# Kernel tuning notes

Measured on AMD Instinct MI355X. Metric: run time of the kernel, lower is better.

Reference implementation:

```python
import jax, jax.numpy as jnp
import numpy as np

B, T, C = 1, 2048, 1024
H, D = 16, 64  # n_head, head_size (n_query_groups == n_head -> plain MHA)


def build_rope_cache(seq_len, n_elem, base=10000):
    theta = 1.0 / (base ** (jnp.arange(0, n_elem, 2, dtype=jnp.float32) / n_elem))
    idx_theta = jnp.outer(jnp.arange(seq_len, dtype=jnp.float32), theta)
    idx_theta = jnp.concatenate([idx_theta, idx_theta], axis=-1)  # torch .repeat(1, 2)
    return jnp.cos(idx_theta), jnp.sin(idx_theta)


def apply_rope(x, cos, sin):
    d = x.shape[-1]
    x1, x2 = x[..., : d // 2], x[..., d // 2 :]
    rotated = jnp.concatenate([-x2, x1], axis=-1)
    return x * cos + rotated * sin


def fastmax_attention(q, k, v):
    """Fastmax: first-order Taylor approx of softmax attention, causal, O(n*d^2).
    score(i,j) = 1 + q_i . k_j (temperature=1, zero RPE, no dropout);
    out_i = sum_{j<=i} score*v_j / sum_{j<=i} score, via causal cumulative sums."""
    n = q.shape[2]
    kcum = jnp.cumsum(k, axis=2)                                       # (B,H,T,D)
    kvcum = jnp.cumsum(jnp.einsum('bhnd,bhne->bhnde', k, v), axis=2)   # (B,H,T,D,D)
    den = jnp.arange(1, n + 1, dtype=q.dtype) + jnp.einsum('bhnd,bhnd->bhn', q, kcum)
    num = jnp.cumsum(v, axis=2) + jnp.einsum('bhnd,bhnde->bhne', q, kvcum)
    return num / den[..., None]


def setup_inputs() -> dict:
    key = jax.random.key(0)
    k1, k2, k3 = jax.random.split(key, 3)
    scale = 0.02
    x = jax.random.normal(k1, (B, T, C), dtype=jnp.float32)
    w_attn = jax.random.normal(k2, (3 * H * D, C), dtype=jnp.float32) * scale
    w_proj = jax.random.normal(k3, (C, H * D), dtype=jnp.float32) * scale
    cos, sin = build_rope_cache(T, D)
    return {"x": x, "w_attn": w_attn, "w_proj": w_proj, "cos": cos, "sin": sin}


def reference(x, w_attn, w_proj, cos, sin):
    Bx, Tx, Cx = x.shape
    qkv = x @ w_attn.T                                  # (B,T,3HD)
    qkv = qkv.reshape(Bx, Tx, H, 3, D).transpose(0, 2, 3, 1, 4)  # (B,H,3,T,D)
    q, k, v = qkv[:, :, 0], qkv[:, :, 1], qkv[:, :, 2]
    q = apply_rope(q, cos, sin)
    k = apply_rope(k, cos, sin)
    y = fastmax_attention(q, k, v)                      # (B,H,T,D)
    y = y.transpose(0, 2, 1, 3).reshape(Bx, Tx, H * D)
    return y @ w_proj.T
```

## Files before the change

### kernel.cpp

```cpp
#include <hip/hip_runtime.h>

#define T_LEN 2048
#define C_DIM 1024
#define H_NUM 16
#define D_DIM 64
#define QKV_N (3 * H_NUM * D_DIM)
#define L_CHK 64
#define NC (T_LEN / L_CHK)

typedef _Float16 h8 __attribute__((ext_vector_type(8)));
typedef _Float16 h4 __attribute__((ext_vector_type(4)));
typedef float f32x4 __attribute__((ext_vector_type(4)));

__global__ __launch_bounds__(256) void split3_f16(
    const float* __restrict__ x, _Float16* __restrict__ xh,
    _Float16* __restrict__ xl, const float* __restrict__ wa,
    _Float16* __restrict__ wah, _Float16* __restrict__ wal,
    const float* __restrict__ wp, _Float16* __restrict__ wph) {
  int i = (blockIdx.x * 256 + threadIdx.x) * 8;
  const float* src;
  _Float16 *dh, *dl = nullptr;
  int base;
  if (i < 2097152) {
    src = x; dh = xh; dl = xl; base = i;
  } else if (i < 2097152 + 3145728) {
    src = wa; dh = wah; dl = wal; base = i - 2097152;
  } else {
    src = wp; dh = wph; base = i - 5242880;
  }
  float4 a = *(const float4*)(src + base);
  float4 b = *(const float4*)(src + base + 4);
  float v[8] = {a.x, a.y, a.z, a.w, b.x, b.y, b.z, b.w};
  h8 hv, lv;
#pragma unroll
  for (int j = 0; j < 8; ++j) {
    float s = v[j] * 64.f;
    _Float16 h = (_Float16)s;
    hv[j] = h;
    lv[j] = (_Float16)(s - (float)h);
  }
  *(h8*)(dh + base) = hv;
  if (dl) *(h8*)(dl + base) = lv;
}

__device__ __forceinline__ void split8(float4 a, float4 b, h8& hi, h8& lo) {
  float v[8] = {a.x, a.y, a.z, a.w, b.x, b.y, b.z, b.w};
#pragma unroll
  for (int m = 0; m < 8; ++m) {
    _Float16 hh = (_Float16)v[m];
    hi[m] = hh;
    lo[m] = (_Float16)(v[m] - (float)hh);
  }
}

template <int BN, bool ROPE, bool SPLIT3>
__global__ __launch_bounds__(256) void gemm_nt_f16(
    const _Float16* __restrict__ Ah, const _Float16* __restrict__ Al,
    const _Float16* __restrict__ Bh, const _Float16* __restrict__ Bl,
    float* __restrict__ C, const float* __restrict__ cosb,
    const float* __restrict__ sinb, _Float16* __restrict__ qh_,
    _Float16* __restrict__ ql_, _Float16* __restrict__ kh_,
    _Float16* __restrict__ kl_, _Float16* __restrict__ kTh_,
    _Float16* __restrict__ kTl_, _Float16* __restrict__ vTh_,
    _Float16* __restrict__ vTl_, int M, int N, int K, float outscale) {
  constexpr int NJ = BN / 32;
  constexpr int NARR = SPLIT3 ? 2 : 1;
  constexpr int GEMM_BYTES = (64 * 64 * 2 + BN * 64 * 2) * NARR;
  constexpr int ROPE_BYTES = ROPE ? (2 * 64 * 64 * 4 + 64 * 64 * 4) : 0;
  constexpr int SMEM_BYTES = GEMM_BYTES > ROPE_BYTES ? GEMM_BYTES : ROPE_BYTES;
  __shared__ __align__(16) char smem[SMEM_BYTES];
  _Float16* sAh = (_Float16*)smem;
  _Float16* sAl = sAh + 64 * 64;
  _Float16* sBh = sAh + 64 * 64 * NARR;
  _Float16* sBl = sBh + BN * 64;
  const int tid = threadIdx.x;
  const int wave = tid >> 6;
  const int lane = tid & 63;
  const int bm = blockIdx.y * 64;
  const int bn = blockIdx.x * BN;
  const int wm = wave >> 1;
  const int wn = wave & 1;
  const int srow = lane >> 3;
  const int sblk = ((lane & 7) ^ srow) * 8;
  const int quad = lane >> 4;
  const int lrow = lane & 15;

  f32x4 acc[2][NJ];
#pragma unroll
  for (int i = 0; i < 2; ++i)
#pragma unroll
    for (int j = 0; j < NJ; ++j) acc[i][j] = (f32x4){0.f, 0.f, 0.f, 0.f};

  for (int k0 = 0; k0 < K; k0 += 64) {
#pragma unroll
    for (int it = 0; it < 2; ++it) {
      const int ch = wave + it * 4;
      const int row = ch * 8 + srow;
      const _Float16* ga = Ah + (size_t)(bm + row) * K + k0 + sblk;
      __builtin_amdgcn_global_load_lds(
          (const __attribute__((address_space(1))) void*)ga,
          (__attribute__((address_space(3))) void*)(sAh + ch * 512), 16, 0, 0);
      if constexpr (SPLIT3) {
        const _Float16* gb = Al + (size_t)(bm + row) * K + k0 + sblk;
        __builtin_amdgcn_global_load_lds(
            (const __attribute__((address_space(1))) void*)gb,
            (__attribute__((address_space(3))) void*)(sAl + ch * 512), 16, 0,
            0);
      }
    }
#pragma unroll
    for (int it = 0; it < BN / 32; ++it) {
      const int ch = wave + it * 4;
      const int row = ch * 8 + srow;
      const _Float16* ga = Bh + (size_t)(bn + row) * K + k0 + sblk;
      __builtin_amdgcn_global_load_lds(
          (const __attribute__((address_space(1))) void*)ga,
          (__attribute__((address_space(3))) void*)(sBh + ch * 512), 16, 0, 0);
      if constexpr (SPLIT3) {
        const _Float16* gb = Bl + (size_t)(bn + row) * K + k0 + sblk;
        __builtin_amdgcn_global_load_lds(
            (const __attribute__((address_space(1))) void*)gb,
            (__attribute__((address_space(3))) void*)(sBl + ch * 512), 16, 0,
            0);
      }
    }
    __syncthreads();
#pragma unroll
    for (int kk = 0; kk < 2; ++kk) {
      h8 ah[2], al[2], bh[NJ], bl[NJ];
#pragma unroll
      for (int i = 0; i < 2; ++i) {
        const int row = wm * 32 + i * 16 + lrow;
        const int ra = row * 64 + (((kk * 4 + quad) ^ (row & 7)) * 8);
        ah[i] = *(const h8*)&sAh[ra];
        if constexpr (SPLIT3) al[i] = *(const h8*)&sAl[ra];
      }
#pragma unroll
      for (int j = 0; j < NJ; ++j) {
        const int row = wn * (BN / 2) + j * 16 + lrow;
        const int rb = row * 64 + (((kk * 4 + quad) ^ (row & 7)) * 8);
        bh[j] = *(const h8*)&sBh[rb];
        if constexpr (SPLIT3) bl[j] = *(const h8*)&sBl[rb];
      }
#pragma unroll
      for (int i = 0; i < 2; ++i)
#pragma unroll
        for (int j = 0; j < NJ; ++j) {
          acc[i][j] = __builtin_amdgcn_mfma_f32_16x16x32_f16(
              ah[i], bh[j], acc[i][j], 0, 0, 0);
          if constexpr (SPLIT3) {
            acc[i][j] = __builtin_amdgcn_mfma_f32_16x16x32_f16(
                ah[i], bl[j], acc[i][j], 0, 0, 0);
            acc[i][j] = __builtin_amdgcn_mfma_f32_16x16x32_f16(
                al[i], bh[j], acc[i][j], 0, 0, 0);
          }
        }
    }
    __syncthreads();
  }
  if constexpr (!ROPE) {
#pragma unroll
    for (int i = 0; i < 2; ++i) {
      const int rbase = bm + wm * 32 + i * 16 + quad * 4;
#pragma unroll
      for (int j = 0; j < NJ; ++j) {
        const int col = bn + wn * (BN / 2) + j * 16 + lrow;
#pragma unroll
        for (int r = 0; r < 4; ++r)
          C[(size_t)(rbase + r) * N + col] = acc[i][j][r] * outscale;
      }
    }
  } else {
    float* cs = (float*)smem;
    float* sn = cs + 4096;
    float* bounce = sn + 4096;
#pragma unroll
    for (int m = 0; m < 4; ++m) {
      int el = (tid + m * 256) * 4;
      *(float4*)&cs[el] = *(const float4*)&cosb[bm * D_DIM + el];
      *(float4*)&sn[el] = *(const float4*)&sinb[bm * D_DIM + el];
    }
    __syncthreads();
    const int colbase = bn + wn * 64;
    const int type = (colbase >> 6) % 3;
    const int head = colbase / 192;
    const size_t hb = (size_t)head * T_LEN * D_DIM;
    float fv[2][4][4];
#pragma unroll
    for (int i = 0; i < 2; ++i)
#pragma unroll
      for (int r = 0; r < 4; ++r) {
        const int tloc = wm * 32 + i * 16 + quad * 4 + r;
#pragma unroll
        for (int j = 0; j < 4; ++j) {
          const int d = j * 16 + lrow;
          float val = acc[i][j][r] * outscale;
          if (type < 2) {
            float rotv =
                ((j < 2) ? -acc[i][j + 2][r] : acc[i][j - 2][r]) * outscale;
            val = val * cs[tloc * D_DIM + d] + rotv * sn[tloc * D_DIM + d];
          }
          fv[i][r][j] = val;
        }
      }
    if (type < 2) {
      _Float16* dh = (type == 0 ? qh_ : kh_) + hb;
      _Float16* dl = (type == 0 ? ql_ : kl_) + hb;
#pragma unroll
      for (int i = 0; i < 2; ++i)
#pragma unroll
        for (int r = 0; r < 4; ++r) {
          const size_t trow =
              (size_t)(bm + wm * 32 + i * 16 + quad * 4 + r) * D_DIM;
#pragma unroll
          for (int j = 0; j < 4; ++j) {
            const int d = j * 16 + lrow;
            float f = fv[i][r][j];
            _Float16 hh = (_Float16)f;
            dh[trow + d] = hh;
            dl[trow + d] = (_Float16)(f - (float)hh);
          }
        }
    }
    const bool doT = (type >= 1);
    _Float16* th = (type == 1 ? kTh_ : vTh_) + hb;
    _Float16* tl = (type == 1 ? kTl_ : vTl_) + hb;
#pragma unroll
    for (int half = 0; half < 2; ++half) {
      __syncthreads();
      if (wn == half && doT) {
#pragma unroll
        for (int i = 0; i < 2; ++i)
#pragma unroll
          for (int r = 0; r < 4; ++r) {
            const int tloc = wm * 32 + i * 16 + quad * 4 + r;
#pragma unroll
            for (int j = 0; j < 4; ++j) {
              const int d = j * 16 + lrow;
              bounce[tloc * 64 + (d ^ tloc)] = fv[i][r][j];
            }
          }
      }
      __syncthreads();
      if (wn == half && doT) {
        const int lt = wm * 64 + lane;
        const int e = lt >> 1;
        const int tg0 = (lt & 1) * 32;
#pragma unroll
        for (int s8 = 0; s8 < 4; ++s8) {
          h8 hv, lv;
#pragma unroll
          for (int s = 0; s < 8; ++s) {
            const int t = tg0 + s8 * 8 + s;
            float f = bounce[t * 64 + (e ^ t)];
            _Float16 hh = (_Float16)f;
            hv[s] = hh;
            lv[s] = (_Float16)(f - (float)hh);
          }
          *(h8*)&th[(size_t)e * T_LEN + bm + tg0 + s8 * 8] = hv;
          *(h8*)&tl[(size_t)e * T_LEN + bm + tg0 + s8 * 8] = lv;
        }
      }
    }
  }
}

__global__ __launch_bounds__(256) void chunk_kvT(
    const _Float16* __restrict__ kTh, const _Float16* __restrict__ kTl,
    const _Float16* __restrict__ vTh, const _Float16* __restrict__ vTl,
    float* __restrict__ kvchunk, float* __restrict__ kschunk,
    float* __restrict__ vschunk) {
  const int blk = blockIdx.x;
  const int h = blk / NC, c = blk % NC;
  const int tid = threadIdx.x;
  const int wave = tid >> 6, lane = tid & 63;
  const int quad = lane >> 4, lrow = lane & 15;
  const size_t hb = (size_t)h * D_DIM * T_LEN;
  const int tb = c * L_CHK;
  h8 avh[2], avl[2];
  {
    const _Float16* pa = vTh + hb + (size_t)(wave * 16 + lrow) * T_LEN + tb +
                         quad * 8;
    const _Float16* pal = vTl + hb + (size_t)(wave * 16 + lrow) * T_LEN + tb +
                          quad * 8;
    avh[0] = *(const h8*)pa;
    avh[1] = *(const h8*)(pa + 32);
    avl[0] = *(const h8*)pal;
    avl[1] = *(const h8*)(pal + 32);
  }
  f32x4 accv[4];
#pragma unroll
  for (int dt = 0; dt < 4; ++dt) accv[dt] = (f32x4){0.f, 0.f, 0.f, 0.f};
#pragma unroll
  for (int dt = 0; dt < 4; ++dt) {
    const _Float16* pb = kTh + hb + (size_t)(dt * 16 + lrow) * T_LEN + tb +
                         quad * 8;
    const _Float16* pbl = kTl + hb + (size_t)(dt * 16 + lrow) * T_LEN + tb +
                          quad * 8;
#pragma unroll
    for (int ks = 0; ks < 2; ++ks) {
      h8 bh = *(const h8*)(pb + ks * 32);
      h8 bl = *(const h8*)(pbl + ks * 32);
      accv[dt] = __builtin_amdgcn_mfma_f32_16x16x32_f16(avh[ks], bh, accv[dt],
                                                        0, 0, 0);
      accv[dt] = __builtin_amdgcn_mfma_f32_16x16x32_f16(avh[ks], bl, accv[dt],
                                                        0, 0, 0);
      accv[dt] = __builtin_amdgcn_mfma_f32_16x16x32_f16(avl[ks], bh, accv[dt],
                                                        0, 0, 0);
    }
  }
  float* ob = kvchunk + (size_t)blk * (D_DIM * D_DIM);
#pragma unroll
  for (int dt = 0; dt < 4; ++dt)
#pragma unroll
    for (int r = 0; r < 4; ++r)
      ob[(wave * 16 + quad * 4 + r) * D_DIM + dt * 16 + lrow] = accv[dt][r];
  if (tid < 64) {
    const _Float16* p = kTh + hb + (size_t)tid * T_LEN + tb;
    const _Float16* pl = kTl + hb + (size_t)tid * T_LEN + tb;
    float s = 0.f;
#pragma unroll
    for (int i = 0; i < 8; ++i) {
      h8 a = *(const h8*)(p + i * 8), b = *(const h8*)(pl + i * 8);
#pragma unroll
      for (int m = 0; m < 8; ++m) s += (float)a[m] + (float)b[m];
    }
    kschunk[(size_t)blk * D_DIM + tid] = s;
  } else if (tid < 128) {
    const int e = tid - 64;
    const _Float16* p = vTh + hb + (size_t)e * T_LEN + tb;
    const _Float16* pl = vTl + hb + (size_t)e * T_LEN + tb;
    float s = 0.f;
#pragma unroll
    for (int i = 0; i < 8; ++i) {
      h8 a = *(const h8*)(p + i * 8), b = *(const h8*)(pl + i * 8);
#pragma unroll
      for (int m = 0; m < 8; ++m) s += (float)a[m] + (float)b[m];
    }
    vschunk[(size_t)blk * D_DIM + e] = s;
  }
}

__global__ __launch_bounds__(256) void scan_fused(
    const float* __restrict__ kvchunk, float* __restrict__ kvpref,
    const float* __restrict__ kschunk, const float* __restrict__ vschunk,
    float* __restrict__ kspref, float* __restrict__ vspref) {
  int b = blockIdx.x;
  int tid = threadIdx.x;
  if (b < 256) {
    int gid = b * 256 + tid;
    int h = gid >> 12;
    int de = gid & 4095;
    float vals[NC];
#pragma unroll
    for (int c = 0; c < NC; ++c)
      vals[c] = kvchunk[((size_t)(h * NC + c) << 12) + de];
    float run = 0.f;
#pragma unroll
    for (int c = 0; c < NC; ++c) {
      kvpref[((size_t)(h * NC + c) << 12) + de] = run;
      run += vals[c];
    }
  } else {
    int gid = (b - 256) * 256 + tid;
    int h = gid >> 6, d = gid & 63;
    float kv_[NC], vv_[NC];
#pragma unroll
    for (int c = 0; c < NC; ++c) {
      size_t idx = (size_t)(h * NC + c) * 64 + d;
      kv_[c] = kschunk[idx];
      vv_[c] = vschunk[idx];
    }
    float rk = 0.f, rv = 0.f;
#pragma unroll
    for (int c = 0; c < NC; ++c) {
      size_t idx = (size_t)(h * NC + c) * 64 + d;
      kspref[idx] = rk;
      vspref[idx] = rv;
      rk += kv_[c];
      rv += vv_[c];
    }
  }
}

__global__ __launch_bounds__(256) void attn_mfma(
    const _Float16* __restrict__ qh, const _Float16* __restrict__ ql,
    const _Float16* __restrict__ kh, const _Float16* __restrict__ kl,
    const _Float16* __restrict__ vTh, const _Float16* __restrict__ vTl,
    const float* __restrict__ kvpref, const float* __restrict__ kspref,
    const float* __restrict__ vspref, _Float16* __restrict__ yh) {
  __shared__ __align__(16) _Float16 sS[2][4][16 * 64];
  const int blk = blockIdx.x;
  const int h = blk / NC, c = blk % NC;
  const int tid = threadIdx.x;
  const int wave = tid >> 6, lane = tid & 63;
  const int quad = lane >> 4, lrow = lane & 15;
  const size_t hb = (size_t)h * T_LEN * D_DIM;
  const size_t hbT = (size_t)h * D_DIM * T_LEN;
  const int t0 = c * L_CHK;
  const f32x4 z4 = {0.f, 0.f, 0.f, 0.f};
  h8 aqh[2], aql[2];
  {
    const _Float16* pq =
        qh + hb + (size_t)(t0 + wave * 16 + lrow) * D_DIM + quad * 8;
    const _Float16* pql =
        ql + hb + (size_t)(t0 + wave * 16 + lrow) * D_DIM + quad * 8;
    aqh[0] = *(const h8*)pq;
    aqh[1] = *(const h8*)(pq + 32);
    aql[0] = *(const h8*)pql;
    aql[1] = *(const h8*)(pql + 32);
  }
  f32x4 sacc[4];
#pragma unroll
  for (int jt = 0; jt < 4; ++jt) sacc[jt] = z4;
#pragma unroll
  for (int jt = 0; jt < 4; ++jt) {
    const _Float16* pk =
        kh + hb + (size_t)(t0 + jt * 16 + lrow) * D_DIM + quad * 8;
    const _Float16* pkl =
        kl + hb + (size_t)(t0 + jt * 16 + lrow) * D_DIM + quad * 8;
#pragma unroll
    for (int ks = 0; ks < 2; ++ks) {
      h8 bh = *(const h8*)(pk + ks * 32);
      h8 bl = *(const h8*)(pkl + ks * 32);
      sacc[jt] = __builtin_amdgcn_mfma_f32_16x16x32_f16(aqh[ks], bh, sacc[jt],
                                                        0, 0, 0);
      sacc[jt] = __builtin_amdgcn_mfma_f32_16x16x32_f16(aqh[ks], bl, sacc[jt],
                                                        0, 0, 0);
      sacc[jt] = __builtin_amdgcn_mfma_f32_16x16x32_f16(aql[ks], bh, sacc[jt],
                                                        0, 0, 0);
    }
  }
  _Float16* shp = &sS[0][wave][0];
  _Float16* slp = &sS[1][wave][0];
#pragma unroll
  for (int jt = 0; jt < 4; ++jt)
#pragma unroll
    for (int r = 0; r < 4; ++r) {
      const int row = quad * 4 + r;
      const int j = jt * 16 + lrow;
      const int rglob = wave * 16 + row;
      float s = (j <= rglob) ? (sacc[jt][r] + 1.f) : 0.f;
      _Float16 hh = (_Float16)s;
      const int adr = row * 64 + ((((j >> 3) ^ (row & 7)) << 3) | (j & 7));
      shp[adr] = hh;
      slp[adr] = (_Float16)(s - (float)hh);
    }
  h8 ash[2], asl[2];
#pragma unroll
  for (int ks = 0; ks < 2; ++ks) {
    const int adr = lrow * 64 + (((ks * 4 + quad) ^ (lrow & 7)) << 3);
    ash[ks] = *(const h8*)&shp[adr];
    asl[ks] = *(const h8*)&slp[adr];
  }
  h8 ones;
#pragma unroll
  for (int m = 0; m < 8; ++m) ones[m] = (_Float16)1.0f;
  f32x4 rs = z4;
#pragma unroll
  for (int ks = 0; ks < 2; ++ks) {
    rs = __builtin_amdgcn_mfma_f32_16x16x32_f16(ash[ks], ones, rs, 0, 0, 0);
    rs = __builtin_amdgcn_mfma_f32_16x16x32_f16(asl[ks], ones, rs, 0, 0, 0);
  }
  f32x4 oacc[4];
#pragma unroll
  for (int et = 0; et < 4; ++et) oacc[et] = z4;
#pragma unroll
  for (int et = 0; et < 4; ++et) {
    const _Float16* pv =
        vTh + hbT + (size_t)(et * 16 + lrow) * T_LEN + t0 + quad * 8;
    const _Float16* pvl =
        vTl + hbT + (size_t)(et * 16 + lrow) * T_LEN + t0 + quad * 8;
#pragma unroll
    for (int ks = 0; ks < 2; ++ks) {
      h8 bh = *(const h8*)(pv + ks * 32);
      h8 bl = *(const h8*)(pvl + ks * 32);
      oacc[et] = __builtin_amdgcn_mfma_f32_16x16x32_f16(ash[ks], bh, oacc[et],
                                                        0, 0, 0);
      oacc[et] = __builtin_amdgcn_mfma_f32_16x16x32_f16(ash[ks], bl, oacc[et],
                                                        0, 0, 0);
      oacc[et] = __builtin_amdgcn_mfma_f32_16x16x32_f16(asl[ks], bh, oacc[et],
                                                        0, 0, 0);
    }
  }
  const float* kvp = kvpref + (size_t)blk * (D_DIM * D_DIM);
#pragma unroll
  for (int et = 0; et < 4; ++et) {
#pragma unroll
    for (int ks = 0; ks < 2; ++ks) {
      const float* pb = kvp + (et * 16 + lrow) * D_DIM + ks * 32 + quad * 8;
      float4 b0 = *(const float4*)pb;
      float4 b1 = *(const float4*)(pb + 4);
      h8 bh, bl;
      split8(b0, b1, bh, bl);
      oacc[et] = __builtin_amdgcn_mfma_f32_16x16x32_f16(aqh[ks], bh, oacc[et],
                                                        0, 0, 0);
      oacc[et] = __builtin_amdgcn_mfma_f32_16x16x32_f16(aqh[ks], bl, oacc[et],
                                                        0, 0, 0);
      oacc[et] = __builtin_amdgcn_mfma_f32_16x16x32_f16(aql[ks], bh, oacc[et],
                                                        0, 0, 0);
    }
  }
  const float* ksp = kspref + (size_t)blk * D_DIM;
  f32x4 kacc = z4;
#pragma unroll
  for (int ks = 0; ks < 2; ++ks) {
    const float* pb = ksp + ks * 32 + quad * 8;
    float4 b0 = *(const float4*)pb;
    float4 b1 = *(const float4*)(pb + 4);
    h8 bh, bl;
    split8(b0, b1, bh, bl);
    kacc = __builtin_amdgcn_mfma_f32_16x16x32_f16(aqh[ks], bh, kacc, 0, 0, 0);
    kacc = __builtin_amdgcn_mfma_f32_16x16x32_f16(aqh[ks], bl, kacc, 0, 0, 0);
    kacc = __builtin_amdgcn_mfma_f32_16x16x32_f16(aql[ks], bh, kacc, 0, 0, 0);
  }
  const float* vsp = vspref + (size_t)blk * D_DIM;
#pragma unroll
  for (int r = 0; r < 4; ++r) {
    const int row = wave * 16 + quad * 4 + r;
    const float den = (float)(c * L_CHK) + rs[r] + kacc[r];
    const float inv = 1.f / den;
    const size_t ybase = (size_t)(t0 + row) * (H_NUM * D_DIM) + h * D_DIM;
#pragma unroll
    for (int et = 0; et < 4; ++et) {
      const int e = et * 16 + lrow;
      const float num = oacc[et][r] + vsp[e];
      yh[ybase + e] = (_Float16)(num * inv);
    }
  }
}

extern "C" void kernel_launch(void* const* d_in, const int* in_sizes, int n_in,
                              void* d_out, int out_size, void* d_ws,
                              size_t ws_size, hipStream_t stream) {
  const float* x = (const float*)d_in[0];
  const float* w_attn = (const float*)d_in[1];
  const float* w_proj = (const float*)d_in[2];
  const float* cosb = (const float*)d_in[3];
  const float* sinb = (const float*)d_in[4];
  float* out = (float*)d_out;

  char* ws = (char*)d_ws;
  const size_t MB = 1048576;
  float* kvchunk = (float*)ws;
  float* kvpref = (float*)(ws + 8 * MB);
  _Float16* qh = (_Float16*)(ws + 16 * MB);
  _Float16* ql = (_Float16*)(ws + 20 * MB);
  _Float16* kh = (_Float16*)(ws + 24 * MB);
  _Float16* kl = (_Float16*)(ws + 28 * MB);
  _Float16* kTh = (_Float16*)(ws + 32 * MB);
  _Float16* kTl = (_Float16*)(ws + 36 * MB);
  _Float16* vTh = (_Float16*)(ws + 40 * MB);
  _Float16* vTl = (_Float16*)(ws + 44 * MB);
  _Float16* xh = (_Float16*)(ws + 48 * MB);
  _Float16* xl = (_Float16*)(ws + 52 * MB);
  _Float16* yh = (_Float16*)(ws + 48 * MB);
  _Float16* wah = (_Float16*)(ws + 56 * MB);
  _Float16* wal = (_Float16*)(ws + 62 * MB);
  float* kschunk = (float*)(ws + 56 * MB);
  float* vschunk = (float*)(ws + 56 * MB + 131072);
  float* kspref = (float*)(ws + 56 * MB + 262144);
  float* vspref = (float*)(ws + 56 * MB + 393216);
  _Float16* wph = (_Float16*)(ws + 68 * MB);

  split3_f16<<<3072, 256, 0, stream>>>(x, xh, xl, w_attn, wah, wal, w_proj,
                                       wph);

  {
    dim3 grid(QKV_N / 128, T_LEN / 64);
    gemm_nt_f16<128, true, true><<<grid, 256, 0, stream>>>(
        xh, xl, wah, wal, nullptr, cosb, sinb, qh, ql, kh, kl, kTh, kTl, vTh,
        vTl, T_LEN, QKV_N, C_DIM, 1.f / 4096.f);
  }
  chunk_kvT<<<H_NUM * NC, 256, 0, stream>>>(kTh, kTl, vTh, vTl, kvchunk,
                                            kschunk, vschunk);
  scan_fused<<<260, 256, 0, stream>>>(kvchunk, kvpref, kschunk, vschunk,
                                      kspref, vspref);
  attn_mfma<<<H_NUM * NC, 256, 0, stream>>>(qh, ql, kh, kl, vTh, vTl, kvpref,
                                            kspref, vspref, yh);
  {
    dim3 grid(C_DIM / 64, T_LEN / 64);
    gemm_nt_f16<64, false, false><<<grid, 256, 0, stream>>>(
        yh, nullptr, wph, nullptr, out, nullptr, nullptr, nullptr, nullptr,
        nullptr, nullptr, nullptr, nullptr, nullptr, nullptr, T_LEN, C_DIM,
        C_DIM, 1.f / 64.f);
  }
}
```

Before: 171.3 us.

## Fuse chunk prefix scan into attention kernel and simplify RoPE epilogue

```diff
diff --git a/kernel.cpp b/kernel.cpp
--- a/kernel.cpp
+++ b/kernel.cpp
@@ -66,7 +66,7 @@
   constexpr int NJ = BN / 32;
   constexpr int NARR = SPLIT3 ? 2 : 1;
   constexpr int GEMM_BYTES = (64 * 64 * 2 + BN * 64 * 2) * NARR;
-  constexpr int ROPE_BYTES = ROPE ? (2 * 64 * 64 * 4 + 64 * 64 * 4) : 0;
+  constexpr int ROPE_BYTES = ROPE ? (2 * 64 * 64 * 4) : 0;
   constexpr int SMEM_BYTES = GEMM_BYTES > ROPE_BYTES ? GEMM_BYTES : ROPE_BYTES;
   __shared__ __align__(16) char smem[SMEM_BYTES];
   _Float16* sAh = (_Float16*)smem;
@@ -171,16 +171,7 @@
       }
     }
   } else {
-    float* cs = (float*)smem;
-    float* sn = cs + 4096;
-    float* bounce = sn + 4096;
-#pragma unroll
-    for (int m = 0; m < 4; ++m) {
-      int el = (tid + m * 256) * 4;
-      *(float4*)&cs[el] = *(const float4*)&cosb[bm * D_DIM + el];
-      *(float4*)&sn[el] = *(const float4*)&sinb[bm * D_DIM + el];
-    }
-    __syncthreads();
+    float* bounce = (float*)smem;
     const int colbase = bn + wn * 64;
     const int type = (colbase >> 6) % 3;
     const int head = colbase / 192;
@@ -198,7 +189,9 @@
           if (type < 2) {
             float rotv =
                 ((j < 2) ? -acc[i][j + 2][r] : acc[i][j - 2][r]) * outscale;
-            val = val * cs[tloc * D_DIM + d] + rotv * sn[tloc * D_DIM + d];
+            const float cs = cosb[(size_t)(bm + tloc) * D_DIM + d];
+            const float sn = sinb[(size_t)(bm + tloc) * D_DIM + d];
+            val = val * cs + rotv * sn;
           }
           fv[i][r][j] = val;
         }
@@ -225,41 +218,38 @@
     const bool doT = (type >= 1);
     _Float16* th = (type == 1 ? kTh_ : vTh_) + hb;
     _Float16* tl = (type == 1 ? kTl_ : vTl_) + hb;
-#pragma unroll
-    for (int half = 0; half < 2; ++half) {
-      __syncthreads();
-      if (wn == half && doT) {
-#pragma unroll
-        for (int i = 0; i < 2; ++i)
-#pragma unroll
-          for (int r = 0; r < 4; ++r) {
-            const int tloc = wm * 32 + i * 16 + quad * 4 + r;
-#pragma unroll
-            for (int j = 0; j < 4; ++j) {
-              const int d = j * 16 + lrow;
-              bounce[tloc * 64 + (d ^ tloc)] = fv[i][r][j];
-            }
+    float* myb = bounce + wn * 4096;
+    if (doT) {
+#pragma unroll
+      for (int i = 0; i < 2; ++i)
+#pragma unroll
+        for (int r = 0; r < 4; ++r) {
+          const int tloc = wm * 32 + i * 16 + quad * 4 + r;
+#pragma unroll
+          for (int j = 0; j < 4; ++j) {
+            const int d = j * 16 + lrow;
+            myb[tloc * 64 + (d ^ tloc)] = fv[i][r][j];
           }
-      }
-      __syncthreads();
-      if (wn == half && doT) {
-        const int lt = wm * 64 + lane;
-        const int e = lt >> 1;
-        const int tg0 = (lt & 1) * 32;
-#pragma unroll
-        for (int s8 = 0; s8 < 4; ++s8) {
-          h8 hv, lv;
-#pragma unroll
-          for (int s = 0; s < 8; ++s) {
-            const int t = tg0 + s8 * 8 + s;
-            float f = bounce[t * 64 + (e ^ t)];
-            _Float16 hh = (_Float16)f;
-            hv[s] = hh;
-            lv[s] = (_Float16)(f - (float)hh);
-          }
-          *(h8*)&th[(size_t)e * T_LEN + bm + tg0 + s8 * 8] = hv;
-          *(h8*)&tl[(size_t)e * T_LEN + bm + tg0 + s8 * 8] = lv;
         }
+    }
+    __syncthreads();
+    if (doT) {
+      const int lt = wm * 64 + lane;
+      const int e = lt >> 1;
+      const int tg0 = (lt & 1) * 32;
+#pragma unroll
+      for (int s8 = 0; s8 < 4; ++s8) {
+        h8 hv, lv;
+#pragma unroll
+        for (int s = 0; s < 8; ++s) {
+          const int t = tg0 + s8 * 8 + s;
+          float f = myb[t * 64 + (e ^ t)];
+          _Float16 hh = (_Float16)f;
+          hv[s] = hh;
+          lv[s] = (_Float16)(f - (float)hh);
+        }
+        *(h8*)&th[(size_t)e * T_LEN + bm + tg0 + s8 * 8] = hv;
+        *(h8*)&tl[(size_t)e * T_LEN + bm + tg0 + s8 * 8] = lv;
       }
     }
   }
@@ -341,55 +331,16 @@
   }
 }
 
-__global__ __launch_bounds__(256) void scan_fused(
-    const float* __restrict__ kvchunk, float* __restrict__ kvpref,
-    const float* __restrict__ kschunk, const float* __restrict__ vschunk,
-    float* __restrict__ kspref, float* __restrict__ vspref) {
-  int b = blockIdx.x;
-  int tid = threadIdx.x;
-  if (b < 256) {
-    int gid = b * 256 + tid;
-    int h = gid >> 12;
-    int de = gid & 4095;
-    float vals[NC];
-#pragma unroll
-    for (int c = 0; c < NC; ++c)
-      vals[c] = kvchunk[((size_t)(h * NC + c) << 12) + de];
-    float run = 0.f;
-#pragma unroll
-    for (int c = 0; c < NC; ++c) {
-      kvpref[((size_t)(h * NC + c) << 12) + de] = run;
-      run += vals[c];
-    }
-  } else {
-    int gid = (b - 256) * 256 + tid;
-    int h = gid >> 6, d = gid & 63;
-    float kv_[NC], vv_[NC];
-#pragma unroll
-    for (int c = 0; c < NC; ++c) {
-      size_t idx = (size_t)(h * NC + c) * 64 + d;
-      kv_[c] = kschunk[idx];
-      vv_[c] = vschunk[idx];
-    }
-    float rk = 0.f, rv = 0.f;
-#pragma unroll
-    for (int c = 0; c < NC; ++c) {
-      size_t idx = (size_t)(h * NC + c) * 64 + d;
-      kspref[idx] = rk;
-      vspref[idx] = rv;
-      rk += kv_[c];
-      rv += vv_[c];
-    }
-  }
-}
-
 __global__ __launch_bounds__(256) void attn_mfma(
     const _Float16* __restrict__ qh, const _Float16* __restrict__ ql,
     const _Float16* __restrict__ kh, const _Float16* __restrict__ kl,
     const _Float16* __restrict__ vTh, const _Float16* __restrict__ vTl,
-    const float* __restrict__ kvpref, const float* __restrict__ kspref,
-    const float* __restrict__ vspref, _Float16* __restrict__ yh) {
+    const float* __restrict__ kvchunk, const float* __restrict__ kschunk,
+    const float* __restrict__ vschunk, _Float16* __restrict__ yh) {
   __shared__ __align__(16) _Float16 sS[2][4][16 * 64];
+  __shared__ __align__(16) float pkv[64 * 68];
+  __shared__ float sks[64];
+  __shared__ float svs[64];
   const int blk = blockIdx.x;
   const int h = blk / NC, c = blk % NC;
   const int tid = threadIdx.x;
@@ -399,6 +350,34 @@
   const size_t hbT = (size_t)h * D_DIM * T_LEN;
   const int t0 = c * L_CHK;
   const f32x4 z4 = {0.f, 0.f, 0.f, 0.f};
+  {
+    f32x4 a0 = z4, a1 = z4, a2 = z4, a3 = z4;
+    const float* base = kvchunk + ((size_t)(h * NC) << 12) + tid * 16;
+    for (int cc = 0; cc < c; ++cc) {
+      const float* p = base + ((size_t)cc << 12);
+      a0 += *(const f32x4*)(p);
+      a1 += *(const f32x4*)(p + 4);
+      a2 += *(const f32x4*)(p + 8);
+      a3 += *(const f32x4*)(p + 12);
+    }
+    const int row = tid >> 2, colb = (tid & 3) * 16;
+    float* d = &pkv[row * 68 + colb];
+    *(f32x4*)(d) = a0;
+    *(f32x4*)(d + 4) = a1;
+    *(f32x4*)(d + 8) = a2;
+    *(f32x4*)(d + 12) = a3;
+  }
+  if (tid < 64) {
+    float s = 0.f;
+    for (int cc = 0; cc < c; ++cc)
+      s += kschunk[(size_t)(h * NC + cc) * D_DIM + tid];
+    sks[tid] = s;
+  } else if (tid < 128) {
+    float s = 0.f;
+    for (int cc = 0; cc < c; ++cc)
+      s += vschunk[(size_t)(h * NC + cc) * D_DIM + (tid - 64)];
+    svs[tid - 64] = s;
+  }
   h8 aqh[2], aql[2];
   {
     const _Float16* pq =
@@ -483,12 +462,12 @@
                                                         0, 0, 0);
     }
   }
-  const float* kvp = kvpref + (size_t)blk * (D_DIM * D_DIM);
+  __syncthreads();
 #pragma unroll
   for (int et = 0; et < 4; ++et) {
 #pragma unroll
     for (int ks = 0; ks < 2; ++ks) {
-      const float* pb = kvp + (et * 16 + lrow) * D_DIM + ks * 32 + quad * 8;
+      const float* pb = &pkv[(et * 16 + lrow) * 68 + ks * 32 + quad * 8];
       float4 b0 = *(const float4*)pb;
       float4 b1 = *(const float4*)(pb + 4);
       h8 bh, bl;
@@ -501,11 +480,10 @@
                                                         0, 0, 0);
     }
   }
-  const float* ksp = kspref + (size_t)blk * D_DIM;
   f32x4 kacc = z4;
 #pragma unroll
   for (int ks = 0; ks < 2; ++ks) {
-    const float* pb = ksp + ks * 32 + quad * 8;
+    const float* pb = &sks[ks * 32 + quad * 8];
     float4 b0 = *(const float4*)pb;
     float4 b1 = *(const float4*)(pb + 4);
     h8 bh, bl;
@@ -514,7 +492,6 @@
     kacc = __builtin_amdgcn_mfma_f32_16x16x32_f16(aqh[ks], bl, kacc, 0, 0, 0);
     kacc = __builtin_amdgcn_mfma_f32_16x16x32_f16(aql[ks], bh, kacc, 0, 0, 0);
   }
-  const float* vsp = vspref + (size_t)blk * D_DIM;
 #pragma unroll
   for (int r = 0; r < 4; ++r) {
     const int row = wave * 16 + quad * 4 + r;
@@ -524,7 +501,7 @@
 #pragma unroll
     for (int et = 0; et < 4; ++et) {
       const int e = et * 16 + lrow;
-      const float num = oacc[et][r] + vsp[e];
+      const float num = oacc[et][r] + svs[e];
       yh[ybase + e] = (_Float16)(num * inv);
     }
   }
@@ -543,7 +520,6 @@
   char* ws = (char*)d_ws;
   const size_t MB = 1048576;
   float* kvchunk = (float*)ws;
-  float* kvpref = (float*)(ws + 8 * MB);
   _Float16* qh = (_Float16*)(ws + 16 * MB);
   _Float16* ql = (_Float16*)(ws + 20 * MB);
   _Float16* kh = (_Float16*)(ws + 24 * MB);
@@ -559,8 +535,6 @@
   _Float16* wal = (_Float16*)(ws + 62 * MB);
   float* kschunk = (float*)(ws + 56 * MB);
   float* vschunk = (float*)(ws + 56 * MB + 131072);
-  float* kspref = (float*)(ws + 56 * MB + 262144);
-  float* vspref = (float*)(ws + 56 * MB + 393216);
   _Float16* wph = (_Float16*)(ws + 68 * MB);
 
   split3_f16<<<3072, 256, 0, stream>>>(x, xh, xl, w_attn, wah, wal, w_proj,
@@ -574,10 +548,8 @@
   }
   chunk_kvT<<<H_NUM * NC, 256, 0, stream>>>(kTh, kTl, vTh, vTl, kvchunk,
                                             kschunk, vschunk);
-  scan_fused<<<260, 256, 0, stream>>>(kvchunk, kvpref, kschunk, vschunk,
-                                      kspref, vspref);
-  attn_mfma<<<H_NUM * NC, 256, 0, stream>>>(qh, ql, kh, kl, vTh, vTl, kvpref,
-                                            kspref, vspref, yh);
+  attn_mfma<<<H_NUM * NC, 256, 0, stream>>>(qh, ql, kh, kl, vTh, vTl, kvchunk,
+                                            kschunk, vschunk, yh);
   {
     dim3 grid(C_DIM / 64, T_LEN / 64);
     gemm_nt_f16<64, false, false><<<grid, 256, 0, stream>>>(
```

Result: slower. 186.3 us (+8.8%).
